# Kernel tuning notes

Measured on AMD Instinct MI355X. Metric: run time of the kernel, lower is better.

## Reference

```python
import jax, jax.numpy as jnp
import numpy as np

N, E = 200_000, 1_000_000
WIDTH, NUM_HEAD = 128, 8
WN, WA = 1, 1            # width_norm, width_act
C = WIDTH * WN           # pre/norm channels
A = WIDTH * WA           # gate/value channels
BOND_SIZE, BAG = 33, 3
EPS = 1e-5               # GroupNorm eps (torch default)


def group_norm(x, groups, eps=EPS):
    # x: [E, C]; normalize per sample per group (affine=False, spatial size 1)
    e, c = x.shape
    xg = x.reshape(e, groups, c // groups)
    m = xg.mean(-1, keepdims=True)
    v = ((xg - m) ** 2).mean(-1, keepdims=True)
    return ((xg - m) * jax.lax.rsqrt(v + eps)).reshape(e, c)


def grouped1x1(x, w, groups):
    # grouped Conv1d with kernel 1, no bias. x: [E, Cin], w: [Cout, Cin//groups]
    e, cin = x.shape
    cout = w.shape[0]
    xg = x.reshape(e, groups, cin // groups)
    wg = w.reshape(groups, cout // groups, cin // groups)
    return jnp.einsum('egi,goi->ego', xg, wg).reshape(e, cout)


def setup_inputs() -> dict:
    key = jax.random.key(0)
    ks = jax.random.split(key, 12)
    x = jax.random.normal(ks[0], (N, WIDTH), jnp.float32)
    # degrees clamped to >= 1 in the original model
    deg = jnp.floor(jax.random.uniform(ks[1], (N,), jnp.float32, 1.0, 8.0))
    edge_idx = jax.random.randint(ks[2], (2, E), 0, N)
    edge_attr = jax.random.randint(ks[3], (E, BAG), 0, BOND_SIZE)
    s_in = 1.0 / np.sqrt(WIDTH)
    s_g = 1.0 / np.sqrt(C // NUM_HEAD)
    s_p = 1.0 / np.sqrt(A)
    pre0_w = jax.random.normal(ks[4], (C, WIDTH), jnp.float32) * s_in
    pre0_b = jnp.zeros((C,), jnp.float32)
    pre1_w = jax.random.normal(ks[5], (C, WIDTH), jnp.float32) * s_in
    pre1_b = jnp.zeros((C,), jnp.float32)
    emb = jax.random.normal(ks[6], (BOND_SIZE, C), jnp.float32)
    emb = emb.at[0].set(0.0)  # padding_idx=0
    gate_w = jax.random.normal(ks[7], (A, C // NUM_HEAD), jnp.float32) * s_g
    value_w = jax.random.normal(ks[8], (A, C // NUM_HEAD), jnp.float32) * s_g
    post_w = jax.random.normal(ks[9], (WIDTH, A), jnp.float32) * s_p
    post_b = jnp.zeros((WIDTH,), jnp.float32)
    degree_param = jnp.full((WIDTH,), -0.01, jnp.float32)
    return {"x": x, "deg": deg, "edge_idx": edge_idx, "edge_attr": edge_attr,
            "pre0_w": pre0_w, "pre0_b": pre0_b, "pre1_w": pre1_w, "pre1_b": pre1_b,
            "emb": emb, "gate_w": gate_w, "value_w": value_w,
            "post_w": post_w, "post_b": post_b, "degree_param": degree_param}


def reference(x, deg, edge_idx, edge_attr, pre0_w, pre0_b, pre1_w, pre1_b,
              emb, gate_w, value_w, post_w, post_b, degree_param):
    n = x.shape[0]
    # conv1x1 projections on nodes, then gather to edges
    h0 = x @ pre0_w.T + pre0_b                      # [N, C]
    h1 = x @ pre1_w.T + pre1_b                      # [N, C]
    xx = h0[edge_idx[0]] + h1[edge_idx[1]]          # [E, C]
    xx = group_norm(xx, NUM_HEAD)
    # EmbeddingBag mean with padding_idx=0 excluded from the mean
    mask = (edge_attr != 0)                          # [E, BAG]
    bag = (emb[edge_attr] * mask[..., None]).sum(1)  # [E, C]
    cnt = jnp.maximum(mask.sum(-1), 1).astype(xx.dtype)
    bag = bag / cnt[:, None]
    # GLU-style gate * value (Dropout is identity at eval)
    gate = jax.nn.relu(grouped1x1(xx + bag, gate_w, NUM_HEAD))  # [E, A]
    val = grouped1x1(xx, value_w, NUM_HEAD)                     # [E, A]
    xx = gate * val
    # scatter-sum back to destination nodes
    agg = jax.ops.segment_sum(xx, edge_idx[1], num_segments=n)  # [N, A]
    out = agg @ post_w.T + post_b                                # [N, WIDTH]
    out = jnp.power(deg[:, None], degree_param) * out
    return out
```

## Files before the change

kernel.cpp:

```cpp
#include <hip/hip_runtime.h>
#include <hip/hip_bf16.h>
#include <hip/hip_fp16.h>


typedef unsigned short u16;
typedef unsigned int   u32;

#define WIDTH 128

#define OFF_W0   0
#define OFF_B0   16384
#define OFF_W1   16512
#define OFF_B1   32896
#define OFF_EMB  33024
#define OFF_GW   37248
#define OFF_VW   39296
#define OFF_PW   41344
#define OFF_PB   57728
#define OFF_DP   57856
#define OFF_WGC  57984
#define OFF_WVC  74368
#define OFF_BGC  90752
#define OFF_BVC  90880
#define OFF_DEG  91008
#define ARENA_PAD 291072

typedef __attribute__((ext_vector_type(8))) short bf16x8;
typedef __attribute__((ext_vector_type(8))) _Float16 f16x8;
typedef __attribute__((ext_vector_type(4))) float f32x4;
typedef __attribute__((ext_vector_type(2))) __fp16 f16x2;

__device__ __forceinline__ float b2f(u16 u){ return __uint_as_float(((u32)u) << 16); }
__device__ __forceinline__ u16   f2b(float f){
  u32 u = __float_as_uint(f);
  u += 0x7fffu + ((u >> 16) & 1u);
  return (u16)(u >> 16);
}
__device__ __forceinline__ u16   f2h(float f){ return __half_as_ushort(__float2half(f)); }
__device__ __forceinline__ float h2f(u16 u){ return __half2float(__ushort_as_half(u)); }

__device__ __forceinline__ f16x2 u2h(u32 u){ union { u32 a; f16x2 b; } c; c.a = u; return c.b; }
__device__ __forceinline__ u32   h2u(f16x2 h){ union { f16x2 b; u32 a; } c; c.b = h; return c.a; }

__device__ __forceinline__ f16x2 pkhfma(f16x2 a, f16x2 b, f16x2 c){
#if __has_builtin(__builtin_elementwise_fma)
  return __builtin_elementwise_fma(a, b, c);
#else
  return a * b + c;
#endif
}

#define DPPADD(s, ctrl) {                                                  \
  const float _t = __uint_as_float((u32)__builtin_amdgcn_update_dpp(       \
      0, (int)__float_as_uint(s), (ctrl), 0xF, 0xF, true));                \
  (s) += _t; }

__device__ __forceinline__ bool is_fp32(const void* degsrc){
  return ((*(const u32*)degsrc) & 0xffffu) == 0u;
}

__device__ __forceinline__ bf16x8 cvt8(float4 a, float4 b){
  bf16x8 r;
  r[0]=(short)f2b(a.x); r[1]=(short)f2b(a.y); r[2]=(short)f2b(a.z); r[3]=(short)f2b(a.w);
  r[4]=(short)f2b(b.x); r[5]=(short)f2b(b.y); r[6]=(short)f2b(b.z); r[7]=(short)f2b(b.w);
  return r;
}
__device__ __forceinline__ f16x8 cvt8h(float4 a, float4 b){
  f16x8 r;
  r[0]=(_Float16)a.x; r[1]=(_Float16)a.y; r[2]=(_Float16)a.z; r[3]=(_Float16)a.w;
  r[4]=(_Float16)b.x; r[5]=(_Float16)b.y; r[6]=(_Float16)b.z; r[7]=(_Float16)b.w;
  return r;
}
__device__ __forceinline__ f16x8 cvtbh(bf16x8 v){
  f16x8 r;
  #pragma unroll
  for (int j = 0; j < 8; ++j) r[j] = (_Float16)b2f((u16)v[j]);
  return r;
}

__device__ __forceinline__ u16 cvt_one(const void* src, int j, bool f32){
  return f32 ? f2b(((const float*)src)[j]) : ((const u16*)src)[j];
}
__device__ __forceinline__ u16 cvt_one_h(const void* src, int j, bool f32){
  return f32 ? f2h(((const float*)src)[j]) : f2h(b2f(((const u16*)src)[j]));
}
__device__ __forceinline__ float read_f(const void* src, int j, bool f32){
  return f32 ? ((const float*)src)[j] : b2f(((const u16*)src)[j]);
}

__global__ void k_init_hist(const void* w0, const void* b0, const void* w1, const void* b1,
                            const void* emb, const void* gw, const void* vw,
                            const void* pw, const void* pb, const void* dp,
                            const void* degsrc, const int* __restrict__ eidx,
                            int* __restrict__ cnt, int E,
                            u16* __restrict__ pb16, u16* __restrict__ gembh,
                            float* __restrict__ gsums, int N)
{
  const bool f32 = is_fp32(degsrc);
  const int nbh = (E + 255) >> 8;
  const int tot_cvt = OFF_WGC + N;
  const int nbc = (tot_cvt + 255) >> 8;
  int b = blockIdx.x;
  const int t = threadIdx.x;

  if (b < nbh) {
    const int e = b * 256 + t;
    if (e < E) atomicAdd(&cnt[eidx[E + e]], 1);
    return;
  }
  b -= nbh;
  if (b < nbc) {
    const int i = b * 256 + t;
    if (i >= tot_cvt) return;
    u16 v; int dsti = i;
    if      (i < OFF_B0 ) v = cvt_one(w0,  i,           f32);
    else if (i < OFF_W1 ) v = cvt_one(b0,  i - OFF_B0,  f32);
    else if (i < OFF_B1 ) v = cvt_one(w1,  i - OFF_W1,  f32);
    else if (i < OFF_EMB) v = cvt_one(b1,  i - OFF_B1,  f32);
    else if (i < OFF_GW ) v = cvt_one(emb, i - OFF_EMB, f32);
    else if (i < OFF_VW ) v = cvt_one_h(gw, i - OFF_GW, f32);
    else if (i < OFF_PW ) v = cvt_one_h(vw, i - OFF_VW, f32);
    else if (i < OFF_PB ) v = cvt_one_h(pw, i - OFF_PW, f32);
    else if (i < OFF_DP ) v = cvt_one(pb,  i - OFF_PB,  f32);
    else if (i < OFF_WGC) v = cvt_one(dp,  i - OFF_DP,  f32);
    else { v = cvt_one(degsrc, i - OFF_WGC, f32); dsti = OFF_DEG + (i - OFF_WGC); }
    pb16[dsti] = v;
    return;
  }
  b -= nbc;
  if (b < 17) {
    const int tid = b * 256 + t;
    if (tid >= 33 * 128) return;
    const int a = tid >> 7, c = tid & 127, g = c >> 4;
    float s = 0.f;
    #pragma unroll
    for (int i = 0; i < 16; ++i)
      s += read_f(gw, c * 16 + i, f32) * read_f(emb, a * WIDTH + g * 16 + i, f32);
    gembh[tid] = f2h(s);
    return;
  }
  b -= 17;
  if (b < 1) {
    if (t < 256) {
      const int c = t & 127;
      const void* src = (t >> 7) ? vw : gw;
      float s = 0.f;
      #pragma unroll
      for (int i = 0; i < 16; ++i) s += read_f(src, c * 16 + i, f32);
      gsums[t] = s;
    }
    return;
  }
  b -= 1;
  if (b < 128) {
    const int tid = b * 256 + t;
    const int m = tid >> 14;
    const int o = (tid >> 7) & 127;
    const int i = tid & 127;
    const void* wsel = m ? vw : gw;
    const int hb = (o >> 4) * 16;
    float s = 0.f;
    #pragma unroll
    for (int j = 0; j < 16; ++j)
      s += read_f(wsel, o * 16 + j, f32) * read_f(w0, (size_t)(hb + j) * 128 + i, f32);
    pb16[(m ? OFF_WVC : OFF_WGC) + o * 128 + i] = f2h(s);
    return;
  }
  if (t < 256) {
    const int m = t >> 7, o = t & 127, hb = (o >> 4) * 16;
    const void* wsel = m ? vw : gw;
    float s = 0.f;
    #pragma unroll
    for (int j = 0; j < 16; ++j)
      s += read_f(wsel, o * 16 + j, f32) * read_f(b0, hb + j, f32);
    pb16[(m ? OFF_BVC : OFF_BGC) + o] = f2h(s);
  }
}

__global__ __launch_bounds__(512, 2) void k_pre_scan1(
    const void* __restrict__ x, const u16* __restrict__ pb16,
    u16* __restrict__ h0, u16* __restrict__ h1,
    u16* __restrict__ ug0, u16* __restrict__ uv0,
    const void* __restrict__ degsrc,
    const int* __restrict__ cnt, int* __restrict__ bsum, int n, int npre)
{
  if ((int)blockIdx.x >= npre) {
    const int t = threadIdx.x, b = (int)blockIdx.x - npre;
    const int i0 = b * 1024 + t * 2;
    int s = 0;
    if (i0     < n) s += cnt[i0];
    if (i0 + 1 < n) s += cnt[i0 + 1];
    __shared__ int sb[512];
    sb[t] = s; __syncthreads();
    for (int d = 256; d > 0; d >>= 1) { if (t < d) sb[t] += sb[t + d]; __syncthreads(); }
    if (t == 0) bsum[b] = sb[0];
    return;
  }

  const int t = threadIdx.x;
  const int lane = t & 63, lid = lane & 15, quad = lane >> 4;
  const int w = t >> 6, mat = w >> 1, c0 = (w & 1) * 64;
  const int node0 = blockIdx.x * 64;
  const bool f32 = is_fp32(degsrc);

  const u16* wsrc; const u16* bsv; u16* dstp;
  if      (mat == 0) { wsrc = pb16 + OFF_W0;  bsv = pb16 + OFF_B0;  dstp = h0;  }
  else if (mat == 1) { wsrc = pb16 + OFF_W1;  bsv = pb16 + OFF_B1;  dstp = h1;  }
  else if (mat == 2) { wsrc = pb16 + OFF_WGC; bsv = pb16 + OFF_BGC; dstp = ug0; }
  else               { wsrc = pb16 + OFF_WVC; bsv = pb16 + OFF_BVC; dstp = uv0; }

  f32x4 acc[4][4];
  #pragma unroll
  for (int nt = 0; nt < 4; ++nt) {
    const u16 braw = bsv[c0 + nt * 16 + lid];
    const float bias = (mat < 2) ? b2f(braw) : h2f(braw);
    #pragma unroll
    for (int mt = 0; mt < 4; ++mt)
      #pragma unroll
      for (int r = 0; r < 4; ++r) acc[mt][nt][r] = bias;
  }

  if (mat < 2) {
    #pragma unroll
    for (int ks = 0; ks < 4; ++ks) {
      bf16x8 a[4], b[4];
      #pragma unroll
      for (int nt = 0; nt < 4; ++nt)
        b[nt] = *(const bf16x8*)(wsrc + (size_t)(c0 + nt * 16 + lid) * WIDTH + ks * 32 + quad * 8);
      if (f32) {
        #pragma unroll
        for (int mt = 0; mt < 4; ++mt) {
          const float4* xr = (const float4*)((const float*)x +
              (size_t)(node0 + mt * 16 + lid) * WIDTH + ks * 32 + quad * 8);
          a[mt] = cvt8(xr[0], xr[1]);
        }
      } else {
        #pragma unroll
        for (int mt = 0; mt < 4; ++mt)
          a[mt] = *(const bf16x8*)((const u16*)x +
              (size_t)(node0 + mt * 16 + lid) * WIDTH + ks * 32 + quad * 8);
      }
      #pragma unroll
      for (int mt = 0; mt < 4; ++mt)
        #pragma unroll
        for (int nt = 0; nt < 4; ++nt)
          acc[mt][nt] = __builtin_amdgcn_mfma_f32_16x16x32_bf16(a[mt], b[nt], acc[mt][nt], 0, 0, 0);
    }
  } else {
    #pragma unroll
    for (int ks = 0; ks < 4; ++ks) {
      f16x8 a[4], b[4];
      #pragma unroll
      for (int nt = 0; nt < 4; ++nt)
        b[nt] = *(const f16x8*)(wsrc + (size_t)(c0 + nt * 16 + lid) * WIDTH + ks * 32 + quad * 8);
      if (f32) {
        #pragma unroll
        for (int mt = 0; mt < 4; ++mt) {
          const float4* xr = (const float4*)((const float*)x +
              (size_t)(node0 + mt * 16 + lid) * WIDTH + ks * 32 + quad * 8);
          a[mt] = cvt8h(xr[0], xr[1]);
        }
      } else {
        #pragma unroll
        for (int mt = 0; mt < 4; ++mt)
          a[mt] = cvtbh(*(const bf16x8*)((const u16*)x +
              (size_t)(node0 + mt * 16 + lid) * WIDTH + ks * 32 + quad * 8));
      }
      #pragma unroll
      for (int mt = 0; mt < 4; ++mt)
        #pragma unroll
        for (int nt = 0; nt < 4; ++nt)
          acc[mt][nt] = __builtin_amdgcn_mfma_f32_16x16x32_f16(a[mt], b[nt], acc[mt][nt], 0, 0, 0);
    }
  }

  #pragma unroll
  for (int mt = 0; mt < 4; ++mt)
    #pragma unroll
    for (int nt = 0; nt < 4; ++nt)
      #pragma unroll
      for (int r = 0; r < 4; ++r)
        dstp[(size_t)(node0 + mt * 16 + quad * 4 + r) * WIDTH + c0 + nt * 16 + lid] =
            f2h(acc[mt][nt][r]);
}

__global__ void k_scan3(const int* __restrict__ cnt, const int* __restrict__ bsum,
                        int* __restrict__ off, int n){
  const int t = threadIdx.x, b = blockIdx.x;
  __shared__ int sp[256];
  int pv = 0;
  for (int j = t; j < b; j += 256) pv += bsum[j];
  sp[t] = pv; __syncthreads();
  for (int d = 128; d > 0; d >>= 1) { if (t < d) sp[t] += sp[t + d]; __syncthreads(); }
  const int bpref = sp[0];

  const int i0 = b * 1024 + t * 4;
  int c[4];
  #pragma unroll
  for (int j = 0; j < 4; ++j) { int i = i0 + j; c[j] = (i < n) ? cnt[i] : 0; }
  int tsum = c[0] + c[1] + c[2] + c[3];
  __shared__ int sb[256];
  sb[t] = tsum; __syncthreads();
  for (int d = 1; d < 256; d <<= 1) {
    int x = (t >= d) ? sb[t - d] : 0;
    __syncthreads();
    sb[t] += x;
    __syncthreads();
  }
  int run = bpref + sb[t] - tsum;
  #pragma unroll
  for (int j = 0; j < 4; ++j) {
    int i = i0 + j;
    if (i < n) off[i] = run;
    run += c[j];
  }
}

__global__ void k_scatter(const int* __restrict__ eidx, const int* __restrict__ eattr,
                          int* __restrict__ off, uint2* __restrict__ sedge, int E){
  const int e = blockIdx.x * 256 + threadIdx.x;
  if (e >= E) return;
  const int dst = eidx[E + e];
  const int pos = atomicAdd(&off[dst], 1);
  const u32 a0 = (u32)eattr[e*3+0], a1 = (u32)eattr[e*3+1], a2 = (u32)eattr[e*3+2];
  u32 cb = (a0 != 0) + (a1 != 0) + (a2 != 0);
  cb = cb ? cb : 1u;
  sedge[pos] = make_uint2((u32)eidx[e], a0 | (a1 << 6) | (a2 << 12) | (cb << 18));
}

__global__ __launch_bounds__(256, 4) void k_agg(
    const u16* __restrict__ h0, const u16* __restrict__ h1,
    const u16* __restrict__ ug0, const u16* __restrict__ uv0,
    const uint2* __restrict__ sedge, const int* __restrict__ off,
    const u16* __restrict__ pb16, const u16* __restrict__ gembh,
    const float* __restrict__ gsums, u16* __restrict__ aggh, const int N)
{
  const int base = ((blockIdx.x * 256 + threadIdx.x) >> 6) * 4;
  if (base >= N) return;
  const int q = threadIdx.x & 63;
  const int c0 = 2 * q;

  u32 gw0[8], gw1[8], vw0[8], vw1[8];
  {
    const u32* g = (const u32*)(pb16 + OFF_GW + (size_t)c0 * 16);
    const u32* v = (const u32*)(pb16 + OFF_VW + (size_t)c0 * 16);
    #pragma unroll
    for (int i = 0; i < 8; ++i) {
      gw0[i] = g[i]; gw1[i] = g[8 + i];
      vw0[i] = v[i]; vw1[i] = v[8 + i];
    }
  }
  const float gs0 = gsums[c0],       gs1 = gsums[c0 + 1];
  const float vs0 = gsums[128 + c0], vs1 = gsums[128 + c0 + 1];

  u32 h1w[4]; int nend[4];
  #pragma unroll
  for (int d = 0; d < 4; ++d) {
    const int dst = min(base + d, N - 1);
    h1w[d]  = *(const u32*)(h1 + (size_t)dst * WIDTH + c0);
    nend[d] = off[dst];
  }
  int ncur = base ? off[base - 1] : 0;
  const int nlast = nend[3];

  u32 hp = 0, ugp = 0, uvp = 0, g0w = 0, g1w = 0, g2w = 0; float pinv = 1.f;
  uint2 edn = make_uint2(0u, 0u);
  if (ncur < nlast) {
    const uint2 e0 = sedge[ncur];
    edn = sedge[min(ncur + 1, nlast - 1)];
    const size_t vo = (size_t)e0.x * WIDTH + c0;
    hp  = *(const u32*)(h0  + vo);
    ugp = *(const u32*)(ug0 + vo);
    uvp = *(const u32*)(uv0 + vo);
    const int a0 = e0.y & 63, a1 = (e0.y >> 6) & 63, a2 = (e0.y >> 12) & 63;
    g0w = *(const u32*)(gembh + (size_t)a0 * WIDTH + c0);
    g1w = *(const u32*)(gembh + (size_t)a1 * WIDTH + c0);
    g2w = *(const u32*)(gembh + (size_t)a2 * WIDTH + c0);
    pinv = __builtin_amdgcn_rcpf((float)((e0.y >> 18) & 3));
  }

  #pragma unroll
  for (int d = 0; d < 4; ++d) {
    const f16x2 h1h = u2h(h1w[d]);

    f16x2 ag0 = u2h(0), ag1 = u2h(0), av0 = u2h(0), av1 = u2h(0);
#define DSTEP(J) {                                                             \
    const f16x2 xj = u2h((u32)__builtin_amdgcn_ds_swizzle(                     \
        (int)h1w[d], 0x18 | ((J) << 5)));                                      \
    ag0 = pkhfma(xj, u2h(gw0[J]), ag0);                                        \
    ag1 = pkhfma(xj, u2h(gw1[J]), ag1);                                        \
    av0 = pkhfma(xj, u2h(vw0[J]), av0);                                        \
    av1 = pkhfma(xj, u2h(vw1[J]), av1); }
    DSTEP(0) DSTEP(1) DSTEP(2) DSTEP(3) DSTEP(4) DSTEP(5) DSTEP(6) DSTEP(7)
#undef DSTEP
    const float ug1d0 = (float)ag0.x + (float)ag0.y;
    const float ug1d1 = (float)ag1.x + (float)ag1.y;
    const float uv1d0 = (float)av0.x + (float)av0.y;
    const float uv1d1 = (float)av1.x + (float)av1.y;

    const int n1 = nend[d];
    float acc0 = 0.f, acc1 = 0.f;

    for (int i = ncur; i < n1; ++i) {
      const u32 hp_c = hp, ug_c = ugp, uv_c = uvp;
      const u32 g0c = g0w, g1c = g1w, g2c = g2w;
      const float inv_c = pinv;
      {
        const uint2 en = edn;
        edn = sedge[min(i + 2, nlast - 1)];
        const size_t vo = (size_t)en.x * WIDTH + c0;
        hp  = *(const u32*)(h0  + vo);
        ugp = *(const u32*)(ug0 + vo);
        uvp = *(const u32*)(uv0 + vo);
        const int a0 = en.y & 63, a1 = (en.y >> 6) & 63, a2 = (en.y >> 12) & 63;
        g0w = *(const u32*)(gembh + (size_t)a0 * WIDTH + c0);
        g1w = *(const u32*)(gembh + (size_t)a1 * WIDTH + c0);
        g2w = *(const u32*)(gembh + (size_t)a2 * WIDTH + c0);
        pinv = __builtin_amdgcn_rcpf((float)((en.y >> 18) & 3));
      }

      const f16x2 xh = u2h(hp_c) + h1h;
      const float x0 = (float)xh.x, x1 = (float)xh.y;

      float s  = x0 + x1;
      float ss = fmaf(x0, x0, x1 * x1);
      DPPADD(s, 0xB1);  DPPADD(ss, 0xB1);
      DPPADD(s, 0x4E);  DPPADD(ss, 0x4E);
      DPPADD(s, 0x141); DPPADD(ss, 0x141);
      const float mean = s * 0.0625f;
      const float var  = fmaf(ss, 0.0625f, -mean * mean);
      const float rs   = __builtin_amdgcn_rsqf(var + 1e-5f);
      const float mrs  = mean * rs;

      const f16x2 bsum3 = u2h(g0c) + u2h(g1c) + u2h(g2c);
      const float bg0 = (float)bsum3.x * inv_c;
      const float bg1 = (float)bsum3.y * inv_c;

      const f16x2 ugh = u2h(ug_c), uvh = u2h(uv_c);
      const float gate0 = fmaf(rs, (float)ugh.x + ug1d0, fmaf(-mrs, gs0, bg0));
      const float gate1 = fmaf(rs, (float)ugh.y + ug1d1, fmaf(-mrs, gs1, bg1));
      const float val0  = fmaf(rs, (float)uvh.x + uv1d0, -mrs * vs0);
      const float val1  = fmaf(rs, (float)uvh.y + uv1d1, -mrs * vs1);
      acc0 = fmaf(fmaxf(gate0, 0.f), val0, acc0);
      acc1 = fmaf(fmaxf(gate1, 0.f), val1, acc1);
    }

    if (base + d < N)
      *(u32*)(aggh + (size_t)(base + d) * WIDTH + c0) =
          h2u(__builtin_amdgcn_cvt_pkrtz(acc0, acc1));
    ncur = n1;
  }
}

__global__ __launch_bounds__(256, 2) void k_post(
    const u16* __restrict__ aggh, const u16* __restrict__ pb16,
    void* __restrict__ out, const void* __restrict__ degsrc)
{
  const int t = threadIdx.x;
  const int lane = t & 63, lid = lane & 15, quad = lane >> 4;
  const int w = t >> 6, c0 = (w & 1) * 64, mh = (w >> 1) * 32;
  const int node0 = blockIdx.x * 64;
  const bool f32o = is_fp32(degsrc);

  f32x4 acc[2][4];
  float dpc[4];
  #pragma unroll
  for (int nt = 0; nt < 4; ++nt) {
    const float bias = b2f(pb16[OFF_PB + c0 + nt * 16 + lid]);
    dpc[nt] = b2f(pb16[OFF_DP + c0 + nt * 16 + lid]);
    #pragma unroll
    for (int mt = 0; mt < 2; ++mt)
      #pragma unroll
      for (int r = 0; r < 4; ++r) acc[mt][nt][r] = bias;
  }

  #pragma unroll
  for (int ks = 0; ks < 4; ++ks) {
    f16x8 a[2], b[4];
    #pragma unroll
    for (int nt = 0; nt < 4; ++nt)
      b[nt] = *(const f16x8*)(pb16 + OFF_PW + (size_t)(c0 + nt * 16 + lid) * WIDTH + ks * 32 + quad * 8);
    #pragma unroll
    for (int mt = 0; mt < 2; ++mt)
      a[mt] = *(const f16x8*)(aggh +
          (size_t)(node0 + mh + mt * 16 + lid) * WIDTH + ks * 32 + quad * 8);
    #pragma unroll
    for (int mt = 0; mt < 2; ++mt)
      #pragma unroll
      for (int nt = 0; nt < 4; ++nt)
        acc[mt][nt] = __builtin_amdgcn_mfma_f32_16x16x32_f16(a[mt], b[nt], acc[mt][nt], 0, 0, 0);
  }

  float logd[2][4];
  #pragma unroll
  for (int mt = 0; mt < 2; ++mt)
    #pragma unroll
    for (int r = 0; r < 4; ++r)
      logd[mt][r] = __logf(b2f(pb16[OFF_DEG + node0 + mh + mt * 16 + quad * 4 + r]));

  #pragma unroll
  for (int mt = 0; mt < 2; ++mt)
    #pragma unroll
    for (int nt = 0; nt < 4; ++nt)
      #pragma unroll
      for (int r = 0; r < 4; ++r) {
        const int node = node0 + mh + mt * 16 + quad * 4 + r;
        const float v = acc[mt][nt][r] * __expf(dpc[nt] * logd[mt][r]);
        if (f32o) ((float*)out)[(size_t)node * WIDTH + c0 + nt * 16 + lid] = v;
        else      ((u16*)out)[(size_t)node * WIDTH + c0 + nt * 16 + lid] = f2b(v);
      }
}

extern "C" void kernel_launch(void* const* d_in, const int* in_sizes, int n_in,
                              void* d_out, int out_size, void* d_ws, size_t ws_size,
                              hipStream_t stream)
{
  (void)n_in; (void)out_size; (void)ws_size;
  const void* x     = d_in[0];
  const void* deg   = d_in[1];
  const int*  eidx  = (const int*)d_in[2];
  const int*  eattr = (const int*)d_in[3];

  const int N = in_sizes[1];
  const int E = in_sizes[2] / 2;

  u16*   aggh = (u16*)d_ws;
  u16*   h1   = aggh + (size_t)N * WIDTH;
  u16*   ug0  = h1   + (size_t)N * WIDTH;
  u16*   uv0  = ug0  + (size_t)N * WIDTH;
  u16*   pb16 = uv0  + (size_t)N * WIDTH;
  u16*   gembh= pb16 + ARENA_PAD;
  float* gsums= (float*)(gembh + 33 * WIDTH);
  int*   cnt  = (int*)(gsums + 256);
  int*   off  = cnt + N;
  int*   bsum = off + N;
  uint2* sedge= (uint2*)(bsum + 1024);
  u16*   h0   = (u16*)d_out;

  const int nbc = (OFF_WGC + N + 255) / 256;
  const int nbh = (E + 255) / 256;

  hipMemsetAsync(cnt, 0, (size_t)N * sizeof(int), stream);

  k_init_hist<<<nbh + nbc + 17 + 1 + 128 + 1, 256, 0, stream>>>(
      d_in[4], d_in[5], d_in[6], d_in[7], d_in[8], d_in[9], d_in[10],
      d_in[11], d_in[12], d_in[13], deg, eidx, cnt, E, pb16, gembh, gsums, N);

  const int npre = N / 64;
  const int nblk = (N + 1023) / 1024;
  k_pre_scan1<<<npre + nblk, 512, 0, stream>>>(
      x, pb16, h0, h1, ug0, uv0, deg, cnt, bsum, N, npre);

  k_scan3  <<<nblk, 256, 0, stream>>>(cnt, bsum, off, N);
  k_scatter<<<nbh, 256, 0, stream>>>(eidx, eattr, off, sedge, E);

  k_agg<<<((size_t)N * 16 + 255) / 256, 256, 0, stream>>>(
      h0, h1, ug0, uv0, sedge, off, pb16, gembh, gsums, aggh, N);

  k_post<<<N / 64, 256, 0, stream>>>(aggh, pb16, d_out, deg);
}
```

Baseline: 679.8 us.

## Fuse sort stages into cooperative kernel, interleave gathered node tables, cache bond embeddings in LDS

The memset, histogram, block-sum, scan and scatter launches become one cooperative kernel that uses grid-wide syncs. The projection kernel now writes h0 and the gate projection interleaved as packed half2 pairs, so each edge gathers them from adjacent words, and the value projection is written to its own buffer. The edge-aggregation kernel loads the 33-entry bond embedding table into shared memory and raises its occupancy bound to 6. This cuts launch count and scattered global traffic, at the cost of grid-sync overhead and a sort that can no longer overlap with the histogram-independent work.

```diff
diff --git a/kernel.cpp b/kernel.cpp
--- a/kernel.cpp
+++ b/kernel.cpp
@@ -1,6 +1,9 @@
 #include <hip/hip_runtime.h>
 #include <hip/hip_bf16.h>
 #include <hip/hip_fp16.h>
+#include <hip/hip_cooperative_groups.h>
+
+namespace cg = cooperative_groups;
 
 
 typedef unsigned short u16;
@@ -88,27 +91,18 @@
   return f32 ? ((const float*)src)[j] : b2f(((const u16*)src)[j]);
 }
 
-__global__ void k_init_hist(const void* w0, const void* b0, const void* w1, const void* b1,
-                            const void* emb, const void* gw, const void* vw,
-                            const void* pw, const void* pb, const void* dp,
-                            const void* degsrc, const int* __restrict__ eidx,
-                            int* __restrict__ cnt, int E,
-                            u16* __restrict__ pb16, u16* __restrict__ gembh,
-                            float* __restrict__ gsums, int N)
+__global__ void k_init(const void* w0, const void* b0, const void* w1, const void* b1,
+                       const void* emb, const void* gw, const void* vw,
+                       const void* pw, const void* pb, const void* dp,
+                       const void* degsrc, u16* __restrict__ pb16,
+                       u16* __restrict__ gembh, float* __restrict__ gsums, int N)
 {
   const bool f32 = is_fp32(degsrc);
-  const int nbh = (E + 255) >> 8;
   const int tot_cvt = OFF_WGC + N;
   const int nbc = (tot_cvt + 255) >> 8;
   int b = blockIdx.x;
   const int t = threadIdx.x;
 
-  if (b < nbh) {
-    const int e = b * 256 + t;
-    if (e < E) atomicAdd(&cnt[eidx[E + e]], 1);
-    return;
-  }
-  b -= nbh;
   if (b < nbc) {
     const int i = b * 256 + t;
     if (i >= tot_cvt) return;
@@ -177,56 +171,114 @@
   }
 }
 
-__global__ __launch_bounds__(512, 2) void k_pre_scan1(
+__global__ __launch_bounds__(256, 1) void k_sort(
+    const int* __restrict__ eidx, const int* __restrict__ eattr,
+    int* __restrict__ cnt, int* __restrict__ bsum, int* __restrict__ off,
+    uint2* __restrict__ sedge, int N, int E)
+{
+  cg::grid_group grid = cg::this_grid();
+  const int T = (int)(gridDim.x * 256);
+  const int tid = (int)(blockIdx.x * 256 + threadIdx.x);
+  const int t = threadIdx.x, b = (int)blockIdx.x;
+  __shared__ int sb[256];
+  __shared__ int sp[256];
+
+  for (int i = tid; i < N; i += T) cnt[i] = 0;
+  grid.sync();
+  for (int e = tid; e < E; e += T) atomicAdd(&cnt[eidx[E + e]], 1);
+  grid.sync();
+
+  const int nblk = (N + 1023) >> 10;
+  if (b < nblk) {
+    const int i0 = b * 1024 + t * 4;
+    int s = 0;
+    #pragma unroll
+    for (int j = 0; j < 4; ++j) { int i = i0 + j; if (i < N) s += cnt[i]; }
+    sb[t] = s; __syncthreads();
+    for (int d = 128; d > 0; d >>= 1) { if (t < d) sb[t] += sb[t + d]; __syncthreads(); }
+    if (t == 0) bsum[b] = sb[0];
+  }
+  grid.sync();
+  if (b < nblk) {
+    int pv = 0;
+    for (int j = t; j < b; j += 256) pv += bsum[j];
+    sp[t] = pv; __syncthreads();
+    for (int d = 128; d > 0; d >>= 1) { if (t < d) sp[t] += sp[t + d]; __syncthreads(); }
+    const int bpref = sp[0];
+    const int i0 = b * 1024 + t * 4;
+    int c[4];
+    #pragma unroll
+    for (int j = 0; j < 4; ++j) { int i = i0 + j; c[j] = (i < N) ? cnt[i] : 0; }
+    int tsum = c[0] + c[1] + c[2] + c[3];
+    __syncthreads();
+    sb[t] = tsum; __syncthreads();
+    for (int d = 1; d < 256; d <<= 1) {
+      int x2 = (t >= d) ? sb[t - d] : 0;
+      __syncthreads(); sb[t] += x2; __syncthreads();
+    }
+    int run = bpref + sb[t] - tsum;
+    #pragma unroll
+    for (int j = 0; j < 4; ++j) { int i = i0 + j; if (i < N) off[i] = run; run += c[j]; }
+  }
+  grid.sync();
+  for (int e = tid; e < E; e += T) {
+    const int dst = eidx[E + e];
+    const int pos = atomicAdd(&off[dst], 1);
+    const u32 a0 = (u32)eattr[e*3+0], a1 = (u32)eattr[e*3+1], a2 = (u32)eattr[e*3+2];
+    u32 cb = (a0 != 0) + (a1 != 0) + (a2 != 0);
+    cb = cb ? cb : 1u;
+    sedge[pos] = make_uint2((u32)eidx[e], a0 | (a1 << 6) | (a2 << 12) | (cb << 18));
+  }
+}
+
+__global__ __launch_bounds__(512, 2) void k_pre(
     const void* __restrict__ x, const u16* __restrict__ pb16,
-    u16* __restrict__ h0, u16* __restrict__ h1,
-    u16* __restrict__ ug0, u16* __restrict__ uv0,
-    const void* __restrict__ degsrc,
-    const int* __restrict__ cnt, int* __restrict__ bsum, int n, int npre)
+    u32* __restrict__ pk0ab, u32* __restrict__ uv0d, u32* __restrict__ h1d,
+    const void* __restrict__ degsrc)
 {
-  if ((int)blockIdx.x >= npre) {
-    const int t = threadIdx.x, b = (int)blockIdx.x - npre;
-    const int i0 = b * 1024 + t * 2;
-    int s = 0;
-    if (i0     < n) s += cnt[i0];
-    if (i0 + 1 < n) s += cnt[i0 + 1];
-    __shared__ int sb[512];
-    sb[t] = s; __syncthreads();
-    for (int d = 256; d > 0; d >>= 1) { if (t < d) sb[t] += sb[t + d]; __syncthreads(); }
-    if (t == 0) bsum[b] = sb[0];
-    return;
-  }
-
   const int t = threadIdx.x;
   const int lane = t & 63, lid = lane & 15, quad = lane >> 4;
   const int w = t >> 6, mat = w >> 1, c0 = (w & 1) * 64;
   const int node0 = blockIdx.x * 64;
   const bool f32 = is_fp32(degsrc);
-
-  const u16* wsrc; const u16* bsv; u16* dstp;
-  if      (mat == 0) { wsrc = pb16 + OFF_W0;  bsv = pb16 + OFF_B0;  dstp = h0;  }
-  else if (mat == 1) { wsrc = pb16 + OFF_W1;  bsv = pb16 + OFF_B1;  dstp = h1;  }
-  else if (mat == 2) { wsrc = pb16 + OFF_WGC; bsv = pb16 + OFF_BGC; dstp = ug0; }
-  else               { wsrc = pb16 + OFF_WVC; bsv = pb16 + OFF_BVC; dstp = uv0; }
-
-  f32x4 acc[4][4];
-  #pragma unroll
-  for (int nt = 0; nt < 4; ++nt) {
-    const u16 braw = bsv[c0 + nt * 16 + lid];
-    const float bias = (mat < 2) ? b2f(braw) : h2f(braw);
-    #pragma unroll
-    for (int mt = 0; mt < 4; ++mt)
-      #pragma unroll
-      for (int r = 0; r < 4; ++r) acc[mt][nt][r] = bias;
-  }
-
-  if (mat < 2) {
+  const bool hp16 = (mat == 1) || (mat == 2);
+
+  const u16* wsrc; const u16* bsv;
+  u32* outp; int slot = 0; bool pkmode = false;
+  if      (mat == 0) { wsrc = pb16 + OFF_W0;  bsv = pb16 + OFF_B0;  outp = pk0ab; slot = 0; pkmode = true; }
+  else if (mat == 1) { wsrc = pb16 + OFF_WGC; bsv = pb16 + OFF_BGC; outp = pk0ab; slot = 1; pkmode = true; }
+  else if (mat == 2) { wsrc = pb16 + OFF_WVC; bsv = pb16 + OFF_BVC; outp = uv0d; }
+  else               { wsrc = pb16 + OFF_W1;  bsv = pb16 + OFF_B1;  outp = h1d; }
+
+  float bias[2][2];
+  #pragma unroll
+  for (int ntp = 0; ntp < 2; ++ntp)
+    #pragma unroll
+    for (int eo = 0; eo < 2; ++eo) {
+      const u16 braw = bsv[c0 + ntp * 32 + 2 * lid + eo];
+      bias[ntp][eo] = hp16 ? h2f(braw) : b2f(braw);
+    }
+
+  f32x4 acc[4][2][2];
+  #pragma unroll
+  for (int mt = 0; mt < 4; ++mt)
+    #pragma unroll
+    for (int ntp = 0; ntp < 2; ++ntp)
+      #pragma unroll
+      for (int eo = 0; eo < 2; ++eo)
+        #pragma unroll
+        for (int r = 0; r < 4; ++r) acc[mt][ntp][eo][r] = bias[ntp][eo];
+
+  if (!hp16) {
     #pragma unroll
     for (int ks = 0; ks < 4; ++ks) {
-      bf16x8 a[4], b[4];
-      #pragma unroll
-      for (int nt = 0; nt < 4; ++nt)
-        b[nt] = *(const bf16x8*)(wsrc + (size_t)(c0 + nt * 16 + lid) * WIDTH + ks * 32 + quad * 8);
+      bf16x8 a[4], bb[2][2];
+      #pragma unroll
+      for (int ntp = 0; ntp < 2; ++ntp)
+        #pragma unroll
+        for (int eo = 0; eo < 2; ++eo)
+          bb[ntp][eo] = *(const bf16x8*)(wsrc +
+              (size_t)(c0 + ntp * 32 + 2 * lid + eo) * WIDTH + ks * 32 + quad * 8);
       if (f32) {
         #pragma unroll
         for (int mt = 0; mt < 4; ++mt) {
@@ -243,16 +295,22 @@
       #pragma unroll
       for (int mt = 0; mt < 4; ++mt)
         #pragma unroll
-        for (int nt = 0; nt < 4; ++nt)
-          acc[mt][nt] = __builtin_amdgcn_mfma_f32_16x16x32_bf16(a[mt], b[nt], acc[mt][nt], 0, 0, 0);
+        for (int ntp = 0; ntp < 2; ++ntp)
+          #pragma unroll
+          for (int eo = 0; eo < 2; ++eo)
+            acc[mt][ntp][eo] = __builtin_amdgcn_mfma_f32_16x16x32_bf16(
+                a[mt], bb[ntp][eo], acc[mt][ntp][eo], 0, 0, 0);
     }
   } else {
     #pragma unroll
     for (int ks = 0; ks < 4; ++ks) {
-      f16x8 a[4], b[4];
-      #pragma unroll
-      for (int nt = 0; nt < 4; ++nt)
-        b[nt] = *(const f16x8*)(wsrc + (size_t)(c0 + nt * 16 + lid) * WIDTH + ks * 32 + quad * 8);
+      f16x8 a[4], bb[2][2];
+      #pragma unroll
+      for (int ntp = 0; ntp < 2; ++ntp)
+        #pragma unroll
+        for (int eo = 0; eo < 2; ++eo)
+          bb[ntp][eo] = *(const f16x8*)(wsrc +
+              (size_t)(c0 + ntp * 32 + 2 * lid + eo) * WIDTH + ks * 32 + quad * 8);
       if (f32) {
         #pragma unroll
         for (int mt = 0; mt < 4; ++mt) {
@@ -269,72 +327,41 @@
       #pragma unroll
       for (int mt = 0; mt < 4; ++mt)
         #pragma unroll
-        for (int nt = 0; nt < 4; ++nt)
-          acc[mt][nt] = __builtin_amdgcn_mfma_f32_16x16x32_f16(a[mt], b[nt], acc[mt][nt], 0, 0, 0);
+        for (int ntp = 0; ntp < 2; ++ntp)
+          #pragma unroll
+          for (int eo = 0; eo < 2; ++eo)
+            acc[mt][ntp][eo] = __builtin_amdgcn_mfma_f32_16x16x32_f16(
+                a[mt], bb[ntp][eo], acc[mt][ntp][eo], 0, 0, 0);
     }
   }
 
   #pragma unroll
   for (int mt = 0; mt < 4; ++mt)
     #pragma unroll
-    for (int nt = 0; nt < 4; ++nt)
-      #pragma unroll
-      for (int r = 0; r < 4; ++r)
-        dstp[(size_t)(node0 + mt * 16 + quad * 4 + r) * WIDTH + c0 + nt * 16 + lid] =
-            f2h(acc[mt][nt][r]);
-}
-
-__global__ void k_scan3(const int* __restrict__ cnt, const int* __restrict__ bsum,
-                        int* __restrict__ off, int n){
-  const int t = threadIdx.x, b = blockIdx.x;
-  __shared__ int sp[256];
-  int pv = 0;
-  for (int j = t; j < b; j += 256) pv += bsum[j];
-  sp[t] = pv; __syncthreads();
-  for (int d = 128; d > 0; d >>= 1) { if (t < d) sp[t] += sp[t + d]; __syncthreads(); }
-  const int bpref = sp[0];
-
-  const int i0 = b * 1024 + t * 4;
-  int c[4];
-  #pragma unroll
-  for (int j = 0; j < 4; ++j) { int i = i0 + j; c[j] = (i < n) ? cnt[i] : 0; }
-  int tsum = c[0] + c[1] + c[2] + c[3];
-  __shared__ int sb[256];
-  sb[t] = tsum; __syncthreads();
-  for (int d = 1; d < 256; d <<= 1) {
-    int x = (t >= d) ? sb[t - d] : 0;
-    __syncthreads();
-    sb[t] += x;
-    __syncthreads();
-  }
-  int run = bpref + sb[t] - tsum;
-  #pragma unroll
-  for (int j = 0; j < 4; ++j) {
-    int i = i0 + j;
-    if (i < n) off[i] = run;
-    run += c[j];
-  }
-}
-
-__global__ void k_scatter(const int* __restrict__ eidx, const int* __restrict__ eattr,
-                          int* __restrict__ off, uint2* __restrict__ sedge, int E){
-  const int e = blockIdx.x * 256 + threadIdx.x;
-  if (e >= E) return;
-  const int dst = eidx[E + e];
-  const int pos = atomicAdd(&off[dst], 1);
-  const u32 a0 = (u32)eattr[e*3+0], a1 = (u32)eattr[e*3+1], a2 = (u32)eattr[e*3+2];
-  u32 cb = (a0 != 0) + (a1 != 0) + (a2 != 0);
-  cb = cb ? cb : 1u;
-  sedge[pos] = make_uint2((u32)eidx[e], a0 | (a1 << 6) | (a2 << 12) | (cb << 18));
-}
-
-__global__ __launch_bounds__(256, 4) void k_agg(
-    const u16* __restrict__ h0, const u16* __restrict__ h1,
-    const u16* __restrict__ ug0, const u16* __restrict__ uv0,
-    const uint2* __restrict__ sedge, const int* __restrict__ off,
-    const u16* __restrict__ pb16, const u16* __restrict__ gembh,
-    const float* __restrict__ gsums, u16* __restrict__ aggh, const int N)
+    for (int r = 0; r < 4; ++r) {
+      const int node = node0 + mt * 16 + quad * 4 + r;
+      #pragma unroll
+      for (int ntp = 0; ntp < 2; ++ntp) {
+        const int p = (c0 >> 1) + ntp * 16 + lid;
+        const u32 pk = h2u(__builtin_amdgcn_cvt_pkrtz(
+            acc[mt][ntp][0][r], acc[mt][ntp][1][r]));
+        if (pkmode) outp[(size_t)node * 128 + p * 2 + slot] = pk;
+        else        outp[(size_t)node * 64 + p] = pk;
+      }
+    }
+}
+
+__global__ __launch_bounds__(256, 6) void k_agg(
+    const u32* __restrict__ pk32, const u32* __restrict__ uv32,
+    const u16* __restrict__ h1, const uint2* __restrict__ sedge,
+    const int* __restrict__ off, const u16* __restrict__ pb16,
+    const u32* __restrict__ gembw, const float* __restrict__ gsums,
+    u16* __restrict__ aggh, const int N)
 {
+  __shared__ u32 gl[2112];
+  for (int j = threadIdx.x; j < 2112; j += 256) gl[j] = gembw[j];
+  __syncthreads();
+
   const int base = ((blockIdx.x * 256 + threadIdx.x) >> 6) * 4;
   if (base >= N) return;
   const int q = threadIdx.x & 63;
@@ -368,14 +395,14 @@
   if (ncur < nlast) {
     const uint2 e0 = sedge[ncur];
     edn = sedge[min(ncur + 1, nlast - 1)];
-    const size_t vo = (size_t)e0.x * WIDTH + c0;
-    hp  = *(const u32*)(h0  + vo);
-    ugp = *(const u32*)(ug0 + vo);
-    uvp = *(const u32*)(uv0 + vo);
+    const u32 po = e0.x * 128u + (u32)(q * 2);
+    hp  = pk32[po];
+    ugp = pk32[po + 1];
+    uvp = uv32[e0.x * 64u + (u32)q];
     const int a0 = e0.y & 63, a1 = (e0.y >> 6) & 63, a2 = (e0.y >> 12) & 63;
-    g0w = *(const u32*)(gembh + (size_t)a0 * WIDTH + c0);
-    g1w = *(const u32*)(gembh + (size_t)a1 * WIDTH + c0);
-    g2w = *(const u32*)(gembh + (size_t)a2 * WIDTH + c0);
+    g0w = gl[a0 * 64 + q];
+    g1w = gl[a1 * 64 + q];
+    g2w = gl[a2 * 64 + q];
     pinv = __builtin_amdgcn_rcpf((float)((e0.y >> 18) & 3));
   }
 
@@ -408,14 +435,14 @@
       {
         const uint2 en = edn;
         edn = sedge[min(i + 2, nlast - 1)];
-        const size_t vo = (size_t)en.x * WIDTH + c0;
-        hp  = *(const u32*)(h0  + vo);
-        ugp = *(const u32*)(ug0 + vo);
-        uvp = *(const u32*)(uv0 + vo);
+        const u32 po = en.x * 128u + (u32)(q * 2);
+        hp  = pk32[po];
+        ugp = pk32[po + 1];
+        uvp = uv32[en.x * 64u + (u32)q];
         const int a0 = en.y & 63, a1 = (en.y >> 6) & 63, a2 = (en.y >> 12) & 63;
-        g0w = *(const u32*)(gembh + (size_t)a0 * WIDTH + c0);
-        g1w = *(const u32*)(gembh + (size_t)a1 * WIDTH + c0);
-        g2w = *(const u32*)(gembh + (size_t)a2 * WIDTH + c0);
+        g0w = gl[a0 * 64 + q];
+        g1w = gl[a1 * 64 + q];
+        g2w = gl[a2 * 64 + q];
         pinv = __builtin_amdgcn_rcpf((float)((en.y >> 18) & 3));
       }
 
@@ -526,36 +553,35 @@
 
   u16*   aggh = (u16*)d_ws;
   u16*   h1   = aggh + (size_t)N * WIDTH;
-  u16*   ug0  = h1   + (size_t)N * WIDTH;
-  u16*   uv0  = ug0  + (size_t)N * WIDTH;
-  u16*   pb16 = uv0  + (size_t)N * WIDTH;
+  u32*   pk0ab= (u32*)(h1 + (size_t)N * WIDTH);
+  u16*   pb16 = (u16*)(pk0ab + (size_t)N * 128);
   u16*   gembh= pb16 + ARENA_PAD;
   float* gsums= (float*)(gembh + 33 * WIDTH);
   int*   cnt  = (int*)(gsums + 256);
   int*   off  = cnt + N;
   int*   bsum = off + N;
   uint2* sedge= (uint2*)(bsum + 1024);
-  u16*   h0   = (u16*)d_out;
+  u32*   uv0d = (u32*)d_out;
 
   const int nbc = (OFF_WGC + N + 255) / 256;
-  const int nbh = (E + 255) / 256;
-
-  hipMemsetAsync(cnt, 0, (size_t)N * sizeof(int), stream);
-
-  k_init_hist<<<nbh + nbc + 17 + 1 + 128 + 1, 256, 0, stream>>>(
+  k_init<<<nbc + 147, 256, 0, stream>>>(
       d_in[4], d_in[5], d_in[6], d_in[7], d_in[8], d_in[9], d_in[10],
-      d_in[11], d_in[12], d_in[13], deg, eidx, cnt, E, pb16, gembh, gsums, N);
-
-  const int npre = N / 64;
-  const int nblk = (N + 1023) / 1024;
-  k_pre_scan1<<<npre + nblk, 512, 0, stream>>>(
-      x, pb16, h0, h1, ug0, uv0, deg, cnt, bsum, N, npre);
-
-  k_scan3  <<<nblk, 256, 0, stream>>>(cnt, bsum, off, N);
-  k_scatter<<<nbh, 256, 0, stream>>>(eidx, eattr, off, sedge, E);
+      d_in[11], d_in[12], d_in[13], deg, pb16, gembh, gsums, N);
+
+  {
+    const int* eidx_a = eidx; const int* eattr_a = eattr;
+    int* cnt_a = cnt; int* bsum_a = bsum; int* off_a = off;
+    uint2* sedge_a = sedge; int N_a = N, E_a = E;
+    void* sargs[8] = { &eidx_a, &eattr_a, &cnt_a, &bsum_a, &off_a,
+                       &sedge_a, &N_a, &E_a };
+    hipLaunchCooperativeKernel((const void*)k_sort, dim3(1024), dim3(256),
+                               sargs, 0, stream);
+  }
+
+  k_pre<<<N / 64, 512, 0, stream>>>(x, pb16, pk0ab, uv0d, (u32*)h1, deg);
 
   k_agg<<<((size_t)N * 16 + 255) / 256, 256, 0, stream>>>(
-      h0, h1, ug0, uv0, sedge, off, pb16, gembh, gsums, aggh, N);
+      pk0ab, uv0d, h1, sedge, off, pb16, (const u32*)gembh, gsums, aggh, N);
 
   k_post<<<N / 64, 256, 0, stream>>>(aggh, pb16, d_out, deg);
 }
```

Measured after the change: 1.064 ms. +56.5%, slower.
